# Kernel tuning notes

Hardware: AMD Instinct MI355X
Metric: run time of the kernel (lower is better)

The kernel has to match this reference:

```python
import jax, jax.numpy as jnp
import numpy as np

DIM = 2048   # token width; == heads*head_dim
H, DH = 16, 128
B, S = 1, 2048
E, K = 4, 2          # routed experts, top-k
HID = 5632           # per-expert SwiGLU hidden: round256(int(2*(4*DIM)/3))
HS = 2816            # shared expert hidden: round256(int(2*(2*DIM)/3))


def setup_inputs() -> dict:
    key = jax.random.key(0)
    ks = jax.random.split(key, 24)
    def g(i, shape, s=0.02):
        return jax.random.normal(ks[i], shape, dtype=jnp.float32) * s
    return {
        "image_tokens": jax.random.normal(ks[0], (B, S, DIM), dtype=jnp.float32),
        "adaln_input": jax.random.normal(ks[1], (B, DIM), dtype=jnp.float32),
        "W_ada": g(2, (DIM, 6 * DIM)), "b_ada": g(3, (6 * DIM,)),
        "Wq": g(4, (DIM, DIM)), "bq": g(5, (DIM,)),
        "Wk": g(6, (DIM, DIM)), "bk": g(7, (DIM,)),
        "Wv": g(8, (DIM, DIM)), "bv": g(9, (DIM,)),
        "q_rms_w": jnp.ones((DIM,), jnp.float32) + g(10, (DIM,)),
        "k_rms_w": jnp.ones((DIM,), jnp.float32) + g(11, (DIM,)),
        "Wo": g(12, (DIM, DIM)), "bo": g(13, (DIM,)),
        "gate_w": g(14, (E, DIM)),
        "We1": g(15, (E, DIM, HID)), "We3": g(16, (E, DIM, HID)), "We2": g(17, (E, HID, DIM)),
        "Ws1": g(18, (DIM, HS)), "Ws3": g(19, (DIM, HS)), "Ws2": g(20, (HS, DIM)),
    }


def _ln(x):  # LayerNorm, elementwise_affine=False, eps=1e-6
    m = jnp.mean(x, -1, keepdims=True)
    v = jnp.var(x, -1, keepdims=True)
    return (x - m) * jax.lax.rsqrt(v + 1e-6)


def _rms(x, w):  # RMSNorm with affine weight, eps=1e-5
    return x * jax.lax.rsqrt(jnp.mean(x * x, -1, keepdims=True) + 1e-5) * w


def reference(image_tokens, adaln_input, W_ada, b_ada, Wq, bq, Wk, bk, Wv, bv,
              q_rms_w, k_rms_w, Wo, bo, gate_w, We1, We3, We2, Ws1, Ws3, Ws2):
    # adaLN: SiLU -> Linear -> 6 chunks, each broadcast as [B,1,dim]
    mod = (jax.nn.silu(adaln_input) @ W_ada + b_ada)[:, None, :]
    sh_msa, sc_msa, g_msa, sh_mlp, sc_mlp, g_mlp = jnp.split(mod, 6, axis=-1)

    # attention branch
    x = _ln(image_tokens) * (1.0 + sc_msa) + sh_msa
    q = _rms(x @ Wq + bq, q_rms_w).reshape(B, S, H, DH)
    k = _rms(x @ Wk + bk, k_rms_w).reshape(B, S, H, DH)
    v = (x @ Wv + bv).reshape(B, S, H, DH)
    att = jax.nn.softmax(jnp.einsum('bihd,bjhd->bhij', q, k) / jnp.sqrt(jnp.float32(DH)), axis=-1)
    o = jnp.einsum('bhij,bjhd->bihd', att, v).reshape(B, S, DIM) @ Wo + bo
    img = g_msa * o + image_tokens

    # MoE SwiGLU FFN branch
    y = _ln(img) * (1.0 + sc_mlp) + sh_mlp
    xf = y.reshape(-1, DIM)                                   # [N, dim]
    scores = jax.nn.softmax(xf @ gate_w.T, axis=-1)           # [N, E]
    tw, ti = jax.lax.top_k(scores, K)                         # no top-k renorm (norm_topk_prob=False)
    comb = jnp.zeros((xf.shape[0], E), xf.dtype).at[jnp.arange(xf.shape[0])[:, None], ti].add(tw)
    h = jax.nn.silu(jnp.einsum('nd,edh->neh', xf, We1)) * jnp.einsum('nd,edh->neh', xf, We3)
    routed = jnp.einsum('neh,ehd,ne->nd', h, We2, comb)
    shared = (jax.nn.silu(xf @ Ws1) * (xf @ Ws3)) @ Ws2
    ff = (routed + shared).reshape(B, S, DIM)

    return g_mlp * ff + img
```

## Files before the change

kernel.cpp:

```cpp
#include <hip/hip_runtime.h>
#include <hip/hip_bf16.h>

typedef unsigned short u16;
typedef __bf16 bf16x8 __attribute__((ext_vector_type(8)));
typedef float f32x4 __attribute__((ext_vector_type(4)));
typedef unsigned short u16x8 __attribute__((ext_vector_type(8)));

constexpr int DIMC = 2048;
constexpr int SEQ = 2048;
constexpr int NHEAD = 16;
constexpr int HDIM = 128;
constexpr int NEXP = 4;
constexpr int HIDC = 5632;
constexpr int HSH = 2816;
constexpr int MOD6 = 6 * DIMC;
constexpr int RSTRIDE = 2304;

static __device__ __forceinline__ u16 f2bf(float f) {
  __hip_bfloat16 b = __float2bfloat16(f);
  return __builtin_bit_cast(u16, b);
}
static __device__ __forceinline__ float bf2f(u16 u) {
  unsigned int x = ((unsigned int)u) << 16;
  return __builtin_bit_cast(float, x);
// ... 52 lines not shown
    u16 h, l;
    splitf(v, h, l);
    size_t idx = (size_t)(c0 + ty + i) * R + r0 + tx;
    outh[idx] = h;
    outl[idx] = l;
  }
}

__global__ __launch_bounds__(256) void k_adaln_p(const float* __restrict__ a, const float* __restrict__ W,
                                                 float* __restrict__ partial) {
  __shared__ float sa[128];
  int tid = threadIdx.x, slice = blockIdx.y;
  if (tid < 128) { float v = a[slice * 128 + tid]; sa[tid] = v * sigf(v); }
  __syncthreads();
  int j = blockIdx.x * 256 + tid;
  float acc = 0.f;
#pragma unroll 4
  for (int d = 0; d < 128; ++d) acc += sa[d] * W[(size_t)(slice * 128 + d) * MOD6 + j];
  partial[(size_t)slice * MOD6 + j] = acc;
}
__global__ __launch_bounds__(256) void k_adaln_r(const float* __restrict__ partial, const float* __restrict__ b,
                                                 float* __restrict__ mod) {
  int j = blockIdx.x * 256 + threadIdx.x;
  float acc = b[j];
#pragma unroll
  for (int s = 0; s < 16; ++s) acc += partial[(size_t)s * MOD6 + j];
  mod[j] = acc;
}

__global__ __launch_bounds__(256) void k_ln_mod_split(const float* __restrict__ X, const float* __restrict__ mod,
                                                      int shOff, int scOff, u16* __restrict__ outh,
                                                      u16* __restrict__ outl) {
  int row = blockIdx.x, tid = threadIdx.x;
  const float4* x4 = (const float4*)(X + (size_t)row * DIMC);
  float4 v0 = x4[tid * 2], v1 = x4[tid * 2 + 1];
  float s = v0.x + v0.y + v0.z + v0.w + v1.x + v1.y + v1.z + v1.w;
  float ss = v0.x * v0.x + v0.y * v0.y + v0.z * v0.z + v0.w * v0.w +
             v1.x * v1.x + v1.y * v1.y + v1.z * v1.z + v1.w * v1.w;
  s = blockSum(s);
  ss = blockSum(ss);
  float mean = s * (1.f / DIMC);
  float var = ss * (1.f / DIMC) - mean * mean;
  float rstd = rsqrtf(var + 1e-6f);
  const float* sh = mod + shOff;
  const float* sc = mod + scOff;
  int c = tid * 8;
  float xv[8] = {v0.x, v0.y, v0.z, v0.w, v1.x, v1.y, v1.z, v1.w};
  u16x8 oh, ol;
#pragma unroll
  for (int e = 0; e < 8; ++e) {
    float v = (xv[e] - mean) * rstd * (1.f + sc[c + e]) + sh[c + e];
    u16 h, l;
    splitf(v, h, l);
    oh[e] = h;
    ol[e] = l;
  }
  *(u16x8*)(outh + (size_t)row * DIMC + c) = oh;
  *(u16x8*)(outl + (size_t)row * DIMC + c) = ol;
}

__global__ __launch_bounds__(256) void k_ln_mod(const float* __restrict__ X, const float* __restrict__ mod,
                                                int shOff, int scOff, u16* __restrict__ out) {
  int row = blockIdx.x, tid = threadIdx.x;
  const float4* x4 = (const float4*)(X + (size_t)row * DIMC);
  float4 v0 = x4[tid * 2], v1 = x4[tid * 2 + 1];
  float s = v0.x + v0.y + v0.z + v0.w + v1.x + v1.y + v1.z + v1.w;
  float ss = v0.x * v0.x + v0.y * v0.y + v0.z * v0.z + v0.w * v0.w +
             v1.x * v1.x + v1.y * v1.y + v1.z * v1.z + v1.w * v1.w;
  s = blockSum(s);
  ss = blockSum(ss);
  float mean = s * (1.f / DIMC);
  float var = ss * (1.f / DIMC) - mean * mean;
  float rstd = rsqrtf(var + 1e-6f);
  const float* sh = mod + shOff;
  const float* sc = mod + scOff;
  int c = tid * 8;
  float xv[8] = {v0.x, v0.y, v0.z, v0.w, v1.x, v1.y, v1.z, v1.w};
  u16x8 o;
#pragma unroll
  for (int e = 0; e < 8; ++e) o[e] = f2bf((xv[e] - mean) * rstd * (1.f + sc[c + e]) + sh[c + e]);
  *(u16x8*)(out + (size_t)row * DIMC + c) = o;
}

__global__ __launch_bounds__(256) void k_rms_split(const float* __restrict__ X, const float* __restrict__ w,
                                                   float scale, u16* __restrict__ outh,
                                                   u16* __restrict__ outl) {
  int row = blockIdx.x, tid = threadIdx.x;
  const float4* x4 = (const float4*)(X + (size_t)row * DIMC);
  float4 v0 = x4[tid * 2], v1 = x4[tid * 2 + 1];
  float ss = v0.x * v0.x + v0.y * v0.y + v0.z * v0.z + v0.w * v0.w +
             v1.x * v1.x + v1.y * v1.y + v1.z * v1.z + v1.w * v1.w;
  ss = blockSum(ss);
  float rstd = rsqrtf(ss * (1.f / DIMC) + 1e-5f) * scale;
  int c = tid * 8;
  float xv[8] = {v0.x, v0.y, v0.z, v0.w, v1.x, v1.y, v1.z, v1.w};
  u16x8 oh, ol;
#pragma unroll
  for (int e = 0; e < 8; ++e) {
    float v = xv[e] * rstd * w[c + e];
    u16 h, l;
    splitf(v, h, l);
    oh[e] = h;
    ol[e] = l;
  }
  *(u16x8*)(outh + (size_t)row * DIMC + c) = oh;
  *(u16x8*)(outl + (size_t)row * DIMC + c) = ol;
}

__global__ __launch_bounds__(256) void k_gate(const float* __restrict__ img, const float* __restrict__ mod,
                                              const float* __restrict__ gw, float* __restrict__ comb) {
  int n = blockIdx.x, tid = threadIdx.x;
  const float4* x4 = (const float4*)(img + (size_t)n * DIMC);
  float4 v0 = x4[tid * 2], v1 = x4[tid * 2 + 1];
  float s = v0.x + v0.y + v0.z + v0.w + v1.x + v1.y + v1.z + v1.w;
  float ss = v0.x * v0.x + v0.y * v0.y + v0.z * v0.z + v0.w * v0.w +
             v1.x * v1.x + v1.y * v1.y + v1.z * v1.z + v1.w * v1.w;
  s = blockSum(s);
  ss = blockSum(ss);
  float mean = s * (1.f / DIMC);
  float var = ss * (1.f / DIMC) - mean * mean;
  float rstd = rsqrtf(var + 1e-6f);
  const float* sh = mod + 3 * DIMC;
  const float* sc = mod + 4 * DIMC;
  int c = tid * 8;
  float xv[8] = {v0.x, v0.y, v0.z, v0.w, v1.x, v1.y, v1.z, v1.w};
  float y[8];
#pragma unroll
  for (int e = 0; e < 8; ++e) y[e] = (xv[e] - mean) * rstd * (1.f + sc[c + e]) + sh[c + e];
  float accs[NEXP];
#pragma unroll
  for (int ex = 0; ex < NEXP; ++ex) {
    float a = 0.f;
#pragma unroll
    for (int e = 0; e < 8; ++e) a += y[e] * gw[(size_t)ex * DIMC + c + e];
    accs[ex] = blockSum(a);
  }
  if (tid == 0) {
    float mx = fmaxf(fmaxf(accs[0], accs[1]), fmaxf(accs[2], accs[3]));
    float ex0 = __expf(accs[0] - mx), ex1 = __expf(accs[1] - mx);
    float ex2 = __expf(accs[2] - mx), ex3 = __expf(accs[3] - mx);
    float inv = 1.f / (ex0 + ex1 + ex2 + ex3);
    float v[4] = {ex0 * inv, ex1 * inv, ex2 * inv, ex3 * inv};
    int i1 = 0;
    for (int e = 1; e < 4; ++e)
      if (v[e] > v[i1]) i1 = e;
    int i2 = -1;
    for (int e = 0; e < 4; ++e) {
      if (e == i1) continue;
      if (i2 < 0 || v[e] > v[i2]) i2 = e;
    }
    for (int e = 0; e < 4; ++e) comb[(size_t)n * 4 + e] = (e == i1 || e == i2) ? v[e] : 0.f;
  }
}

__global__ __launch_bounds__(256) void k_route(const float* __restrict__ comb, int* __restrict__ gidx,
                                               float* __restrict__ cw, int* __restrict__ Mpad) {
  int wid = threadIdx.x >> 6, lane = threadIdx.x & 63;
  int base = 0;
  for (int c = 0; c < SEQ; c += 64) {
    int n = c + lane;
    float w = comb[(size_t)n * NEXP + wid];
    bool sel = w > 0.f;
    unsigned long long mask = __ballot(sel);
    int pos = __popcll(mask & ((1ull << lane) - 1ull));
    if (sel) {
      gidx[wid * RSTRIDE + base + pos] = n;
      cw[wid * RSTRIDE + base + pos] = w;
    }
    base += __popcll(mask);
  }
  int padded = (base + 127) & ~127;
  for (int i = base + lane; i < padded; i += 64) {
    gidx[wid * RSTRIDE + i] = -1;
    cw[wid * RSTRIDE + i] = 0.f;
  }
  if (lane == 0) Mpad[wid] = padded;
}

template <int MODE>
__global__ __launch_bounds__(256, 2) void k_gemm(const u16* __restrict__ A, const u16* __restrict__ BT,
                                                 int M, int N, int K, float* __restrict__ Cf,
                                                 u16* __restrict__ Cb, const u16* __restrict__ h1) {
  __shared__ __align__(16) u16 As[2][8192], Bs[2][8192];
  const int tid = threadIdx.x, wid = tid >> 6, lane = tid & 63;
  const int l16 = lane & 15, g = lane >> 4;
  const int wr = wid >> 1, wc = wid & 1;
  const int m0 = blockIdx.y * 128, n0 = blockIdx.x * 128;
  const int srow = lane >> 2, scol = (lane & 3) * 8;
  const u16* aS0 = A + (size_t)(m0 + wid * 32 + srow) * K + scol;
  const u16* aS1 = aS0 + (size_t)16 * K;
  const u16* bS0 = BT + (size_t)(n0 + wid * 32 + srow) * K + scol;
  const u16* bS1 = bS0 + (size_t)16 * K;

  const f32x4 zero4 = {0.f, 0.f, 0.f, 0.f};
  f32x4 acc[4][4];
#pragma unroll
  for (int mi = 0; mi < 4; ++mi)
#pragma unroll
    for (int ni = 0; ni < 4; ++ni) acc[mi][ni] = zero4;

  auto stage = [&](int b, int k0) {
    gload16(aS0 + k0, &As[b][wid * 1024]);
    gload16(aS1 + k0, &As[b][wid * 1024 + 512]);
    gload16(aS0 + k0 + 32, &As[b][4096 + wid * 1024]);
    gload16(aS1 + k0 + 32, &As[b][4096 + wid * 1024 + 512]);
    gload16(bS0 + k0, &Bs[b][wid * 1024]);
    gload16(bS1 + k0, &Bs[b][wid * 1024 + 512]);
    gload16(bS0 + k0 + 32, &Bs[b][4096 + wid * 1024]);
    gload16(bS1 + k0 + 32, &Bs[b][4096 + wid * 1024 + 512]);
  };
  auto compute = [&](int b) {
#pragma unroll
    for (int hh = 0; hh < 2; ++hh) {
      const u16* Asrc = &As[b][hh * 4096];
      const u16* Bsrc = &Bs[b][hh * 4096];
      bf16x8 af[4], bfr[4];
#pragma unroll
      for (int mi = 0; mi < 4; ++mi)
        af[mi] = *(const bf16x8*)(&Asrc[(wr * 64 + mi * 16 + l16) * 32 + g * 8]);
#pragma unroll
      for (int ni = 0; ni < 4; ++ni)
        bfr[ni] = *(const bf16x8*)(&Bsrc[(wc * 64 + ni * 16 + l16) * 32 + g * 8]);
#pragma unroll
      for (int mi = 0; mi < 4; ++mi)
#pragma unroll
        for (int ni = 0; ni < 4; ++ni)
          acc[mi][ni] = __builtin_amdgcn_mfma_f32_16x16x32_bf16(af[mi], bfr[ni], acc[mi][ni], 0, 0, 0);
    }
  };

  stage(0, 0);
  __syncthreads();
  for (int k0 = 0; k0 < K; k0 += 128) {
    if (k0 + 64 < K) stage(1, k0 + 64);
    compute(0);
    __syncthreads();
    if (k0 + 128 < K) stage(0, k0 + 128);
    compute(1);
    __syncthreads();
  }

#pragma unroll
  for (int mi = 0; mi < 4; ++mi) {
#pragma unroll
    for (int ni = 0; ni < 4; ++ni) {
      const int col = n0 + wc * 64 + ni * 16 + l16;
#pragma unroll
      for (int r = 0; r < 4; ++r) {
        const int row = m0 + wr * 64 + mi * 16 + g * 4 + r;
        const size_t idx = (size_t)row * N + col;
        float v = acc[mi][ni][r];
        if constexpr (MODE == 0) {
          Cf[idx] = v;
        } else if constexpr (MODE == 1) {
          Cb[idx] = f2bf(v);
        } else {
          float hv = bf2f(h1[idx]);
          float sw = hv * sigf(hv);
          Cb[idx] = f2bf(sw * v);
        }
      }
    }
  }
}

template <int RM>
__global__ __launch_bounds__(256, 2) void k_gemmR(const u16* __restrict__ A0, size_t az,
                                                  const u16* __restrict__ BT0, size_t bz, int N, int K,
                                                  const int* __restrict__ gidx0,
                                                  const float* __restrict__ cw0,
                                                  const int* __restrict__ Mp0, u16* __restrict__ Cb0,
                                                  size_t cz, const u16* __restrict__ h10,
                                                  float* __restrict__ ff) {
  const int z = blockIdx.z;
  const int* gidxE = gidx0 + (size_t)z * RSTRIDE;
  const int m0 = blockIdx.y * 128;
  if (m0 >= Mp0[z]) return;
  const float* cwE = cw0 + (size_t)z * RSTRIDE;
  const u16* A = A0 + (size_t)z * az;
  const u16* BT = BT0 + (size_t)z * bz;
  u16* Cb = Cb0 + (size_t)z * cz;
  const u16* h1 = h10 + (size_t)z * cz;

  __shared__ __align__(16) u16 As[2][8192], Bs[2][8192];
  const int tid = threadIdx.x, wid = tid >> 6, lane = tid & 63;
  const int l16 = lane & 15, g = lane >> 4;
  const int wr = wid >> 1, wc = wid & 1;
  const int n0 = blockIdx.x * 128;
  const int srow = lane >> 2, scol = (lane & 3) * 8;
  const int slot0 = m0 + wid * 32 + srow;
  int row0, row1;
  if constexpr (RM == 2) {
    row0 = slot0;
    row1 = slot0 + 16;
  } else {
    int t0 = gidxE[slot0], t1 = gidxE[slot0 + 16];
    row0 = t0 < 0 ? 0 : t0;
    row1 = t1 < 0 ? 0 : t1;
  }
  const u16* aS0 = A + (size_t)row0 * K + scol;
  const u16* aS1 = A + (size_t)row1 * K + scol;
  const u16* bS0 = BT + (size_t)(n0 + wid * 32 + srow) * K + scol;
  const u16* bS1 = bS0 + (size_t)16 * K;

  const f32x4 zero4 = {0.f, 0.f, 0.f, 0.f};
  f32x4 acc[4][4];
#pragma unroll
  for (int mi = 0; mi < 4; ++mi)
#pragma unroll
    for (int ni = 0; ni < 4; ++ni) acc[mi][ni] = zero4;

  auto stage = [&](int b, int k0) {
    gload16(aS0 + k0, &As[b][wid * 1024]);
    gload16(aS1 + k0, &As[b][wid * 1024 + 512]);
    gload16(aS0 + k0 + 32, &As[b][4096 + wid * 1024]);
    gload16(aS1 + k0 + 32, &As[b][4096 + wid * 1024 + 512]);
    gload16(bS0 + k0, &Bs[b][wid * 1024]);
    gload16(bS1 + k0, &Bs[b][wid * 1024 + 512]);
    gload16(bS0 + k0 + 32, &Bs[b][4096 + wid * 1024]);
    gload16(bS1 + k0 + 32, &Bs[b][4096 + wid * 1024 + 512]);
  };
  auto compute = [&](int b) {
#pragma unroll
    for (int hh = 0; hh < 2; ++hh) {
      const u16* Asrc = &As[b][hh * 4096];
      const u16* Bsrc = &Bs[b][hh * 4096];
      bf16x8 af[4], bfr[4];
#pragma unroll
      for (int mi = 0; mi < 4; ++mi)
        af[mi] = *(const bf16x8*)(&Asrc[(wr * 64 + mi * 16 + l16) * 32 + g * 8]);
#pragma unroll
      for (int ni = 0; ni < 4; ++ni)
        bfr[ni] = *(const bf16x8*)(&Bsrc[(wc * 64 + ni * 16 + l16) * 32 + g * 8]);
#pragma unroll
      for (int mi = 0; mi < 4; ++mi)
#pragma unroll
        for (int ni = 0; ni < 4; ++ni)
          acc[mi][ni] = __builtin_amdgcn_mfma_f32_16x16x32_bf16(af[mi], bfr[ni], acc[mi][ni], 0, 0, 0);
    }
  };

  stage(0, 0);
  __syncthreads();
  for (int k0 = 0; k0 < K; k0 += 128) {
    if (k0 + 64 < K) stage(1, k0 + 64);
    compute(0);
    __syncthreads();
    if (k0 + 128 < K) stage(0, k0 + 128);
    compute(1);
    __syncthreads();
  }

#pragma unroll
  for (int mi = 0; mi < 4; ++mi) {
#pragma unroll
    for (int ni = 0; ni < 4; ++ni) {
      const int col = n0 + wc * 64 + ni * 16 + l16;
#pragma unroll
      for (int r = 0; r < 4; ++r) {
        const int slot = m0 + wr * 64 + mi * 16 + g * 4 + r;
        const size_t idx = (size_t)slot * N + col;
        float v = acc[mi][ni][r];
        if constexpr (RM == 0) {
          Cb[idx] = f2bf(v);
        } else if constexpr (RM == 1) {
          float hv = bf2f(h1[idx]);
          float sw = hv * sigf(hv);
          Cb[idx] = f2bf(sw * v * cwE[slot]);
        } else {
          int t = gidxE[slot];
          if (t >= 0) ff[(size_t)t * N + col] += v;
        }
      }
    }
  }
}

template <int MODE>
__global__ __launch_bounds__(256, 2) void k_gemm3s(const u16* __restrict__ Ahg, const u16* __restrict__ Alg,
                                                   const u16* __restrict__ Bhg, const u16* __restrict__ Blg,
                                                   int M, int N, int K, float* __restrict__ Cf,
                                                   u16* __restrict__ Ch, u16* __restrict__ Cl,
                                                   const float* __restrict__ bias,
                                                   const float* __restrict__ gvec,
                                                   const float* __restrict__ resid) {
  __shared__ __align__(16) u16 Ahs[2][4096], Als[2][4096], Bhs[2][4096], Bls[2][4096];
  const int tid = threadIdx.x, wid = tid >> 6, lane = tid & 63;
  const int l16 = lane & 15, g = lane >> 4;
  const int wr = wid >> 1, wc = wid & 1;
  const int m0 = blockIdx.y * 128, n0 = blockIdx.x * 128;
  const int srow = lane >> 2, scol = (lane & 3) * 8;
  const size_t aOff0 = (size_t)(m0 + wid * 32 + srow) * K + scol;
  const size_t aOff1 = aOff0 + (size_t)16 * K;
  const size_t bOff0 = (size_t)(n0 + wid * 32 + srow) * K + scol;
  const size_t bOff1 = bOff0 + (size_t)16 * K;

  const f32x4 zero4 = {0.f, 0.f, 0.f, 0.f};
  f32x4 acc[4][4];
#pragma unroll
  for (int mi = 0; mi < 4; ++mi)
#pragma unroll
    for (int ni = 0; ni < 4; ++ni) acc[mi][ni] = zero4;

  auto stage = [&](int b, int k0) {
    gload16(Ahg + aOff0 + k0, &Ahs[b][wid * 1024]);
    gload16(Ahg + aOff1 + k0, &Ahs[b][wid * 1024 + 512]);
    gload16(Alg + aOff0 + k0, &Als[b][wid * 1024]);
    gload16(Alg + aOff1 + k0, &Als[b][wid * 1024 + 512]);
    gload16(Bhg + bOff0 + k0, &Bhs[b][wid * 1024]);
    gload16(Bhg + bOff1 + k0, &Bhs[b][wid * 1024 + 512]);
    gload16(Blg + bOff0 + k0, &Bls[b][wid * 1024]);
    gload16(Blg + bOff1 + k0, &Bls[b][wid * 1024 + 512]);
  };
  auto compute = [&](int b) {
    bf16x8 bhf[4], blf[4];
#pragma unroll
    for (int ni = 0; ni < 4; ++ni) {
      bhf[ni] = *(const bf16x8*)(&Bhs[b][(wc * 64 + ni * 16 + l16) * 32 + g * 8]);
      blf[ni] = *(const bf16x8*)(&Bls[b][(wc * 64 + ni * 16 + l16) * 32 + g * 8]);
    }
#pragma unroll
    for (int mi = 0; mi < 4; ++mi) {
      bf16x8 ahf = *(const bf16x8*)(&Ahs[b][(wr * 64 + mi * 16 + l16) * 32 + g * 8]);
      bf16x8 alf = *(const bf16x8*)(&Als[b][(wr * 64 + mi * 16 + l16) * 32 + g * 8]);
#pragma unroll
      for (int ni = 0; ni < 4; ++ni) {
        acc[mi][ni] = __builtin_amdgcn_mfma_f32_16x16x32_bf16(alf, bhf[ni], acc[mi][ni], 0, 0, 0);
        acc[mi][ni] = __builtin_amdgcn_mfma_f32_16x16x32_bf16(ahf, blf[ni], acc[mi][ni], 0, 0, 0);
        acc[mi][ni] = __builtin_amdgcn_mfma_f32_16x16x32_bf16(ahf, bhf[ni], acc[mi][ni], 0, 0, 0);
      }
    }
  };

  stage(0, 0);
  __syncthreads();
  for (int k0 = 0; k0 < K; k0 += 64) {
    if (k0 + 32 < K) stage(1, k0 + 32);
    compute(0);
    __syncthreads();
    if (k0 + 64 < K) stage(0, k0 + 64);
    compute(1);
    __syncthreads();
  }

#pragma unroll
  for (int mi = 0; mi < 4; ++mi) {
#pragma unroll
    for (int ni = 0; ni < 4; ++ni) {
      const int col = n0 + wc * 64 + ni * 16 + l16;
      float bv = bias ? bias[col] : 0.f;
#pragma unroll
      for (int r = 0; r < 4; ++r) {
        const int row = m0 + wr * 64 + mi * 16 + g * 4 + r;
        float v = acc[mi][ni][r] + bv;
        if constexpr (MODE == 0) {
          Cf[(size_t)row * N + col] = v;
        } else if constexpr (MODE == 2) {
          Cf[(size_t)row * N + col] = v * gvec[col] + resid[(size_t)row * N + col];
        } else {
          u16 h, l;
          splitf(v, h, l);
          Ch[(size_t)col * M + row] = h;
          Cl[(size_t)col * M + row] = l;
        }
      }
    }
  }
}

__global__ __launch_bounds__(256, 3) void k_flash3(const u16* __restrict__ qh_g, const u16* __restrict__ ql_g,
                                                   const u16* __restrict__ kh_g, const u16* __restrict__ kl_g,
                                                   const u16* __restrict__ vth_g, const u16* __restrict__ vtl_g,
                                                   u16* __restrict__ oh_g, u16* __restrict__ ol_g) {
  __shared__ __align__(16) u16 Kh[4096], Kl[4096], Vh[128 * 40], Vl[128 * 40];
  __shared__ __align__(16) u16 Pah[4][16 * 40], Pal[4][16 * 40];
  const int tid = threadIdx.x, wid = tid >> 6, lane = tid & 63;
  const int l16 = lane & 15, g = lane >> 4;
  const int h = blockIdx.y;
  const int r0 = blockIdx.x * 64 + wid * 16;
  const size_t hOff = (size_t)h * HDIM;

  bf16x8 qfh[4], qfl[4];
#pragma unroll
  for (int kc = 0; kc < 4; ++kc) {
    const size_t qo = (size_t)(r0 + l16) * DIMC + hOff + kc * 32 + g * 8;
    qfh[kc] = *(const bf16x8*)(qh_g + qo);
    qfl[kc] = *(const bf16x8*)(ql_g + qo);
  }

  const int kr = tid >> 3, ke0 = (tid & 7) * 16;
  const int kswz = (kr & 7) << 4;
  const int kc0 = (ke0 * 2) ^ kswz, kc1 = (ke0 * 2 + 16) ^ kswz;
  char* khp = (char*)Kh + kr * 256;
  char* klp = (char*)Kl + kr * 256;
  const size_t kOff = (size_t)kr * DIMC + hOff + ke0;
  const int vr = tid >> 1, ve0 = (tid & 1) * 16;
  char* vhp = (char*)Vh + vr * 80 + ve0 * 2;
  char* vlp = (char*)Vl + vr * 80 + ve0 * 2;
  const size_t vOff = (size_t)(hOff + vr) * SEQ + ve0;

  u16x8 kH0, kH1, kL0, kL1, vH0, vH1, vL0, vL1;
  kH0 = *(const u16x8*)(kh_g + kOff);
  kH1 = *(const u16x8*)(kh_g + kOff + 8);
  kL0 = *(const u16x8*)(kl_g + kOff);
  kL1 = *(const u16x8*)(kl_g + kOff + 8);
  vH0 = *(const u16x8*)(vth_g + vOff);
  vH1 = *(const u16x8*)(vth_g + vOff + 8);
  vL0 = *(const u16x8*)(vtl_g + vOff);
  vL1 = *(const u16x8*)(vtl_g + vOff + 8);

  const f32x4 zero4 = {0.f, 0.f, 0.f, 0.f};
  f32x4 oacc[8];
#pragma unroll
  for (int db = 0; db < 8; ++db) oacc[db] = zero4;
  float mr[4], lr[4];
#pragma unroll
  for (int r = 0; r < 4; ++r) {
    mr[r] = -3.0e38f;
    lr[r] = 0.f;
  }

  for (int j0 = 0; j0 < SEQ; j0 += 32) {
    __syncthreads();
    *(u16x8*)(khp + kc0) = kH0;
    *(u16x8*)(khp + kc1) = kH1;
    *(u16x8*)(klp + kc0) = kL0;
    *(u16x8*)(klp + kc1) = kL1;
    *(u16x8*)(vhp) = vH0;
    *(u16x8*)(vhp + 16) = vH1;
    *(u16x8*)(vlp) = vL0;
    *(u16x8*)(vlp + 16) = vL1;
    __syncthreads();
    if (j0 + 32 < SEQ) {
      const size_t ko = kOff + (size_t)(j0 + 32) * DIMC;
      const size_t vo = vOff + j0 + 32;
      kH0 = *(const u16x8*)(kh_g + ko);
      kH1 = *(const u16x8*)(kh_g + ko + 8);
      kL0 = *(const u16x8*)(kl_g + ko);
      kL1 = *(const u16x8*)(kl_g + ko + 8);
      vH0 = *(const u16x8*)(vth_g + vo);
      vH1 = *(const u16x8*)(vth_g + vo + 8);
      vL0 = *(const u16x8*)(vtl_g + vo);
      vL1 = *(const u16x8*)(vtl_g + vo + 8);
    }
    f32x4 s0 = zero4, s1 = zero4;
    __builtin_amdgcn_s_setprio(1);
#pragma unroll
    for (int kc = 0; kc < 4; ++kc) {
      const int cb = (kc * 64 + g * 16) ^ ((l16 & 7) << 4);
      bf16x8 kh0 = *(const bf16x8*)((char*)Kh + l16 * 256 + cb);
// ... 41 lines not shown
      oacc[db] = __builtin_amdgcn_mfma_f32_16x16x32_bf16(pfl, vh, oacc[db], 0, 0, 0);
      oacc[db] = __builtin_amdgcn_mfma_f32_16x16x32_bf16(pfh, vl, oacc[db], 0, 0, 0);
      oacc[db] = __builtin_amdgcn_mfma_f32_16x16x32_bf16(pfh, vh, oacc[db], 0, 0, 0);
    }
    __builtin_amdgcn_s_setprio(0);
  }
#pragma unroll
  for (int r = 0; r < 4; ++r) {
#pragma unroll
    for (int m = 1; m < 16; m <<= 1) lr[r] += __shfl_xor(lr[r], m);
    lr[r] = 1.f / lr[r];
  }
#pragma unroll
  for (int db = 0; db < 8; ++db)
#pragma unroll
    for (int r = 0; r < 4; ++r) {
      float v = oacc[db][r] * lr[r];
      u16 hh, ll;
      splitf(v, hh, ll);
      const size_t idx = (size_t)(r0 + g * 4 + r) * DIMC + hOff + db * 16 + l16;
      oh_g[idx] = hh;
      ol_g[idx] = ll;
    }
}

__global__ __launch_bounds__(256) void k_final(const float* __restrict__ ff, const float* img,
                                               const float* __restrict__ mod, float* out) {
  const float4* gm = (const float4*)(mod + 5 * DIMC);
  const int total = SEQ * DIMC / 4;
  const int stride = gridDim.x * blockDim.x;
  for (int i = blockIdx.x * blockDim.x + threadIdx.x; i < total; i += stride) {
    int col4 = i & (DIMC / 4 - 1);
    float4 gv = gm[col4];
    float4 fv = ((const float4*)ff)[i];
    float4 iv = ((const float4*)img)[i];
    float4 ov;
    ov.x = gv.x * fv.x + iv.x;
    ov.y = gv.y * fv.y + iv.y;
    ov.z = gv.z * fv.z + iv.z;
    ov.w = gv.w * fv.w + iv.w;
    ((float4*)out)[i] = ov;
  }
}

extern "C" void kernel_launch(void* const* d_in, const int* in_sizes, int n_in, void* d_out, int out_size,
                              void* d_ws, size_t ws_size, hipStream_t stream) {
  (void)in_sizes; (void)n_in; (void)out_size; (void)ws_size;
  const float* image_tokens = (const float*)d_in[0];
  const float* adaln_input = (const float*)d_in[1];
  const float* W_ada = (const float*)d_in[2];
  const float* b_ada = (const float*)d_in[3];
  const float* Wq = (const float*)d_in[4];
  const float* bq = (const float*)d_in[5];
  const float* Wk = (const float*)d_in[6];
  const float* bk = (const float*)d_in[7];
  const float* Wv = (const float*)d_in[8];
  const float* bv = (const float*)d_in[9];
  const float* q_rms_w = (const float*)d_in[10];
  const float* k_rms_w = (const float*)d_in[11];
  const float* Wo = (const float*)d_in[12];
  const float* bo = (const float*)d_in[13];
  const float* gate_w = (const float*)d_in[14];
  const float* We1 = (const float*)d_in[15];
  const float* We3 = (const float*)d_in[16];
  const float* We2 = (const float*)d_in[17];
  const float* Ws1 = (const float*)d_in[18];
  const float* Ws3 = (const float*)d_in[19];
  const float* Ws2 = (const float*)d_in[20];

  char* cur = (char*)d_ws;
  auto alloc = [&](size_t n) {
    char* p = cur;
    cur += (n + 255) & ~(size_t)255;
    return p;
  };
  float* modv = (float*)alloc((size_t)MOD6 * 4);
  float* adap = (float*)alloc((size_t)16 * MOD6 * 4);
  float* comb = (float*)alloc((size_t)SEQ * NEXP * 4);
  int* gidx = (int*)alloc((size_t)NEXP * RSTRIDE * 4);
  float* cw = (float*)alloc((size_t)NEXP * RSTRIDE * 4);
  int* Mpad = (int*)alloc((size_t)NEXP * 4);
  u16* xh = (u16*)alloc((size_t)SEQ * DIMC * 2);
  u16* xl = (u16*)alloc((size_t)SEQ * DIMC * 2);
  u16* wTh = (u16*)alloc((size_t)DIMC * DIMC * 2);
  u16* wTl = (u16*)alloc((size_t)DIMC * DIMC * 2);
  float* tf = (float*)alloc((size_t)SEQ * DIMC * 4);
  u16* qhb = (u16*)alloc((size_t)SEQ * DIMC * 2);
  u16* qlb = (u16*)alloc((size_t)SEQ * DIMC * 2);
  u16* khb = (u16*)alloc((size_t)SEQ * DIMC * 2);
  u16* klb = (u16*)alloc((size_t)SEQ * DIMC * 2);
  u16* vth = (u16*)alloc((size_t)SEQ * DIMC * 2);
  u16* vtl = (u16*)alloc((size_t)SEQ * DIMC * 2);
  u16* aoh = (u16*)alloc((size_t)SEQ * DIMC * 2);
  u16* aol = (u16*)alloc((size_t)SEQ * DIMC * 2);
  u16* x_act = (u16*)alloc((size_t)SEQ * DIMC * 2);
  float* ff = (float*)alloc((size_t)SEQ * DIMC * 4);
  float* img = (float*)d_out;
  u16* wbufE = xh;
  u16* H1G2 = (u16*)((char*)xh + (size_t)2 * HIDC * DIMC * 2);
  const size_t BZ = (size_t)HIDC * DIMC;
  const size_t CZ = (size_t)RSTRIDE * HIDC;
  u16* wbufS = wbufE;
  u16* H1Gs = H1G2;

  dim3 blk(256);
  auto gemm3s = [&](int mode, const u16* Ah, const u16* Al, int M, int N, int K, float* Cf, u16* Ch,
                    u16* Cl, const float* bias, const float* gv, const float* resid) {
    dim3 grid(N / 128, M / 128);
    switch (mode) {
      case 0:
        k_gemm3s<0><<<grid, blk, 0, stream>>>(Ah, Al, wTh, wTl, M, N, K, Cf, Ch, Cl, bias, gv, resid);
        break;
      case 2:
        k_gemm3s<2><<<grid, blk, 0, stream>>>(Ah, Al, wTh, wTl, M, N, K, Cf, Ch, Cl, bias, gv, resid);
        break;
      default:
        k_gemm3s<6><<<grid, blk, 0, stream>>>(Ah, Al, wTh, wTl, M, N, K, Cf, Ch, Cl, bias, gv, resid);
        break;
    }
  };

  k_adaln_p<<<dim3(MOD6 / 256, 16), blk, 0, stream>>>(adaln_input, W_ada, adap);
  k_adaln_r<<<dim3(MOD6 / 256), blk, 0, stream>>>(adap, b_ada, modv);

  k_ln_mod_split<<<dim3(SEQ), blk, 0, stream>>>(image_tokens, modv, 0, DIMC, xh, xl);
  k_transpose_s<<<dim3(DIMC / 32, DIMC / 32), blk, 0, stream>>>(Wq, wTh, wTl, DIMC, DIMC, DIMC);
  gemm3s(0, xh, xl, SEQ, DIMC, DIMC, tf, nullptr, nullptr, bq, nullptr, nullptr);
  k_rms_split<<<dim3(SEQ), blk, 0, stream>>>(tf, q_rms_w, 0.08838834764831845f, qhb, qlb);
  k_transpose_s<<<dim3(DIMC / 32, DIMC / 32), blk, 0, stream>>>(Wk, wTh, wTl, DIMC, DIMC, DIMC);
  gemm3s(0, xh, xl, SEQ, DIMC, DIMC, tf, nullptr, nullptr, bk, nullptr, nullptr);
  k_rms_split<<<dim3(SEQ), blk, 0, stream>>>(tf, k_rms_w, 1.f, khb, klb);
  k_transpose_s<<<dim3(DIMC / 32, DIMC / 32), blk, 0, stream>>>(Wv, wTh, wTl, DIMC, DIMC, DIMC);
  gemm3s(6, xh, xl, SEQ, DIMC, DIMC, nullptr, vth, vtl, bv, nullptr, nullptr);
  k_flash3<<<dim3(SEQ / 64, NHEAD), blk, 0, stream>>>(qhb, qlb, khb, klb, vth, vtl, aoh, aol);
  k_transpose_s<<<dim3(DIMC / 32, DIMC / 32), blk, 0, stream>>>(Wo, wTh, wTl, DIMC, DIMC, DIMC);
  gemm3s(2, aoh, aol, SEQ, DIMC, DIMC, img, nullptr, nullptr, bo, modv + 2 * DIMC, image_tokens);

  k_ln_mod<<<dim3(SEQ), blk, 0, stream>>>(img, modv, 3 * DIMC, 4 * DIMC, x_act);
  k_gate<<<dim3(SEQ), blk, 0, stream>>>(img, modv, gate_w, comb);
  k_route<<<dim3(1), blk, 0, stream>>>(comb, gidx, cw, Mpad);

  k_transpose<<<dim3(HSH / 32, DIMC / 32), blk, 0, stream>>>(Ws1, wbufS, DIMC, HSH, HSH, 0, 0);
  k_gemm<1><<<dim3(HSH / 128, SEQ / 128), blk, 0, stream>>>(x_act, wbufS, SEQ, HSH, DIMC, nullptr,
                                                            H1Gs, nullptr);
  k_transpose<<<dim3(HSH / 32, DIMC / 32), blk, 0, stream>>>(Ws3, wbufS, DIMC, HSH, HSH, 0, 0);
  k_gemm<3><<<dim3(HSH / 128, SEQ / 128), blk, 0, stream>>>(x_act, wbufS, SEQ, HSH, DIMC, nullptr,
                                                            H1Gs, H1Gs);
  k_transpose<<<dim3(DIMC / 32, HSH / 32), blk, 0, stream>>>(Ws2, wbufS, HSH, DIMC, DIMC, 0, 0);
  k_gemm<0><<<dim3(DIMC / 128, SEQ / 128), blk, 0, stream>>>(H1Gs, wbufS, SEQ, DIMC, HSH, ff,
                                                             nullptr, nullptr);

  const size_t WE = (size_t)DIMC * HIDC;
  for (int p = 0; p < 2; ++p) {
    const int e0 = p * 2;
    const int* ge = gidx + e0 * RSTRIDE;
    const float* ce = cw + e0 * RSTRIDE;
    const int* me = Mpad + e0;
    k_transpose<<<dim3(HIDC / 32, DIMC / 32, 2), blk, 0, stream>>>(We1 + (size_t)e0 * WE, wbufE,
                                                                   DIMC, HIDC, HIDC, WE, BZ);
    k_gemmR<0><<<dim3(HIDC / 128, SEQ / 128, 2), blk, 0, stream>>>(x_act, 0, wbufE, BZ, HIDC, DIMC,
                                                                   ge, ce, me, H1G2, CZ, H1G2, nullptr);
    k_transpose<<<dim3(HIDC / 32, DIMC / 32, 2), blk, 0, stream>>>(We3 + (size_t)e0 * WE, wbufE,
                                                                   DIMC, HIDC, HIDC, WE, BZ);
    k_gemmR<1><<<dim3(HIDC / 128, SEQ / 128, 2), blk, 0, stream>>>(x_act, 0, wbufE, BZ, HIDC, DIMC,
                                                                   ge, ce, me, H1G2, CZ, H1G2, nullptr);
    k_transpose<<<dim3(DIMC / 32, HIDC / 32, 2), blk, 0, stream>>>(We2 + (size_t)e0 * WE, wbufE,
                                                                   HIDC, DIMC, DIMC, WE, BZ);
    for (int z = 0; z < 2; ++z) {
      k_gemmR<2><<<dim3(DIMC / 128, SEQ / 128, 1), blk, 0, stream>>>(
          H1G2 + (size_t)z * CZ, 0, wbufE + (size_t)z * BZ, 0, DIMC, HIDC, gidx + (e0 + z) * RSTRIDE,
          cw + (e0 + z) * RSTRIDE, Mpad + e0 + z, H1G2, 0, H1G2, ff);
    }
  }

  k_final<<<dim3(1024), blk, 0, stream>>>(ff, img, modv, (float*)d_out);
}
```

Measured before the change: 1.715 ms.

## Fuse QKV projection into one GEMM and fuse SwiGLU up-projections into dual-B GEMM

Transposes Wq/Wk/Wv into one concatenated buffer and runs a single 3-split GEMM over N=3*DIM with a per-column-block bias select. RMS norms then read strided rows from the fused output, and V is transposed by a separate kernel. The gate/up GEMMs for both the shared and routed experts become one kernel that loads A once and accumulates against W1 and W3 together, applying SiLU-multiply and the routing weight in the epilogue. This saves A reloads, kernel launches and the bf16 H1 round trip through memory. In exchange the fused kernel keeps twice the accumulators and drops double-buffered staging, which may cut occupancy and latency hiding, and the QKV output buffer triples in size.

```diff
diff --git a/kernel.cpp b/kernel.cpp
--- a/kernel.cpp
+++ b/kernel.cpp
@@ -158,11 +158,11 @@
   *(u16x8*)(out + (size_t)row * DIMC + c) = o;
 }
 
-__global__ __launch_bounds__(256) void k_rms_split(const float* __restrict__ X, const float* __restrict__ w,
-                                                   float scale, u16* __restrict__ outh,
-                                                   u16* __restrict__ outl) {
+__global__ __launch_bounds__(256) void k_rms_split(const float* __restrict__ X, int ldin,
+                                                   const float* __restrict__ w, float scale,
+                                                   u16* __restrict__ outh, u16* __restrict__ outl) {
   int row = blockIdx.x, tid = threadIdx.x;
-  const float4* x4 = (const float4*)(X + (size_t)row * DIMC);
+  const float4* x4 = (const float4*)(X + (size_t)row * ldin);
   float4 v0 = x4[tid * 2], v1 = x4[tid * 2 + 1];
   float ss = v0.x * v0.x + v0.y * v0.y + v0.z * v0.z + v0.w * v0.w +
              v1.x * v1.x + v1.y * v1.y + v1.z * v1.z + v1.w * v1.w;
@@ -253,10 +253,8 @@
   if (lane == 0) Mpad[wid] = padded;
 }
 
-template <int MODE>
-__global__ __launch_bounds__(256, 2) void k_gemm(const u16* __restrict__ A, const u16* __restrict__ BT,
-                                                 int M, int N, int K, float* __restrict__ Cf,
-                                                 u16* __restrict__ Cb, const u16* __restrict__ h1) {
+__global__ __launch_bounds__(256, 2) void k_gemmD(const u16* __restrict__ A, const u16* __restrict__ BT,
+                                                  int M, int N, int K, float* __restrict__ Cf) {
   __shared__ __align__(16) u16 As[2][8192], Bs[2][8192];
   const int tid = threadIdx.x, wid = tid >> 6, lane = tid & 63;
   const int l16 = lane & 15, g = lane >> 4;
@@ -317,47 +315,132 @@
   }
 
 #pragma unroll
-  for (int mi = 0; mi < 4; ++mi) {
+  for (int mi = 0; mi < 4; ++mi)
 #pragma unroll
     for (int ni = 0; ni < 4; ++ni) {
       const int col = n0 + wc * 64 + ni * 16 + l16;
 #pragma unroll
       for (int r = 0; r < 4; ++r) {
         const int row = m0 + wr * 64 + mi * 16 + g * 4 + r;
-        const size_t idx = (size_t)row * N + col;
-        float v = acc[mi][ni][r];
-        if constexpr (MODE == 0) {
-          Cf[idx] = v;
-        } else if constexpr (MODE == 1) {
-          Cb[idx] = f2bf(v);
-        } else {
-          float hv = bf2f(h1[idx]);
-          float sw = hv * sigf(hv);
-          Cb[idx] = f2bf(sw * v);
+        Cf[(size_t)row * N + col] = acc[mi][ni][r];
+      }
+    }
+}
+
+template <int GATH>
+__global__ __launch_bounds__(256, 2) void k_gemmUP(const u16* __restrict__ A, const u16* __restrict__ B1T0,
+                                                   const u16* __restrict__ B3T0, size_t bz, int N, int K,
+                                                   const int* __restrict__ gidx0,
+                                                   const float* __restrict__ cw0,
+                                                   const int* __restrict__ Mp0, u16* __restrict__ G0,
+                                                   size_t cz) {
+  const int z = blockIdx.z;
+  const int m0 = blockIdx.y * 128;
+  const int* gidxE = nullptr;
+  const float* cwE = nullptr;
+  if constexpr (GATH) {
+    if (m0 >= Mp0[z]) return;
+    gidxE = gidx0 + (size_t)z * RSTRIDE;
+    cwE = cw0 + (size_t)z * RSTRIDE;
+  }
+  const u16* B1T = B1T0 + (size_t)z * bz;
+  const u16* B3T = B3T0 + (size_t)z * bz;
+  u16* G = G0 + (size_t)z * cz;
+
+  __shared__ __align__(16) u16 As[8192], B1s[8192], B3s[8192];
+  const int tid = threadIdx.x, wid = tid >> 6, lane = tid & 63;
+  const int l16 = lane & 15, g = lane >> 4;
+  const int wr = wid >> 1, wc = wid & 1;
+  const int n0 = blockIdx.x * 128;
+  const int srow = lane >> 2, scol = (lane & 3) * 8;
+  const int slot0 = m0 + wid * 32 + srow;
+  int row0, row1;
+  if constexpr (GATH) {
+    int t0 = gidxE[slot0], t1 = gidxE[slot0 + 16];
+    row0 = t0 < 0 ? 0 : t0;
+    row1 = t1 < 0 ? 0 : t1;
+  } else {
+    row0 = slot0;
+    row1 = slot0 + 16;
+  }
+  const u16* aS0 = A + (size_t)row0 * K + scol;
+  const u16* aS1 = A + (size_t)row1 * K + scol;
+  const u16* b1S0 = B1T + (size_t)(n0 + wid * 32 + srow) * K + scol;
+  const u16* b1S1 = b1S0 + (size_t)16 * K;
+  const u16* b3S0 = B3T + (size_t)(n0 + wid * 32 + srow) * K + scol;
+  const u16* b3S1 = b3S0 + (size_t)16 * K;
+
+  const f32x4 zero4 = {0.f, 0.f, 0.f, 0.f};
+  f32x4 acc1[4][4], acc3[4][4];
+#pragma unroll
+  for (int mi = 0; mi < 4; ++mi)
+#pragma unroll
+    for (int ni = 0; ni < 4; ++ni) {
+      acc1[mi][ni] = zero4;
+      acc3[mi][ni] = zero4;
+    }
+
+  for (int k0 = 0; k0 < K; k0 += 64) {
+    __syncthreads();
+    gload16(aS0 + k0, &As[wid * 1024]);
+    gload16(aS1 + k0, &As[wid * 1024 + 512]);
+    gload16(aS0 + k0 + 32, &As[4096 + wid * 1024]);
+    gload16(aS1 + k0 + 32, &As[4096 + wid * 1024 + 512]);
+    gload16(b1S0 + k0, &B1s[wid * 1024]);
+    gload16(b1S1 + k0, &B1s[wid * 1024 + 512]);
+    gload16(b1S0 + k0 + 32, &B1s[4096 + wid * 1024]);
+    gload16(b1S1 + k0 + 32, &B1s[4096 + wid * 1024 + 512]);
+    gload16(b3S0 + k0, &B3s[wid * 1024]);
+    gload16(b3S1 + k0, &B3s[wid * 1024 + 512]);
+    gload16(b3S0 + k0 + 32, &B3s[4096 + wid * 1024]);
+    gload16(b3S1 + k0 + 32, &B3s[4096 + wid * 1024 + 512]);
+    __syncthreads();
+#pragma unroll
+    for (int hh = 0; hh < 2; ++hh) {
+      const u16* Asrc = &As[hh * 4096];
+      const u16* B1src = &B1s[hh * 4096];
+      const u16* B3src = &B3s[hh * 4096];
+      bf16x8 af[4], b1f[4], b3f[4];
+#pragma unroll
+      for (int mi = 0; mi < 4; ++mi)
+        af[mi] = *(const bf16x8*)(&Asrc[(wr * 64 + mi * 16 + l16) * 32 + g * 8]);
+#pragma unroll
+      for (int ni = 0; ni < 4; ++ni) {
+        b1f[ni] = *(const bf16x8*)(&B1src[(wc * 64 + ni * 16 + l16) * 32 + g * 8]);
+        b3f[ni] = *(const bf16x8*)(&B3src[(wc * 64 + ni * 16 + l16) * 32 + g * 8]);
+      }
+#pragma unroll
+      for (int mi = 0; mi < 4; ++mi)
+#pragma unroll
+        for (int ni = 0; ni < 4; ++ni) {
+          acc1[mi][ni] = __builtin_amdgcn_mfma_f32_16x16x32_bf16(af[mi], b1f[ni], acc1[mi][ni], 0, 0, 0);
+          acc3[mi][ni] = __builtin_amdgcn_mfma_f32_16x16x32_bf16(af[mi], b3f[ni], acc3[mi][ni], 0, 0, 0);
         }
+    }
+  }
+
+#pragma unroll
+  for (int mi = 0; mi < 4; ++mi)
+#pragma unroll
+    for (int ni = 0; ni < 4; ++ni) {
+      const int col = n0 + wc * 64 + ni * 16 + l16;
+#pragma unroll
+      for (int r = 0; r < 4; ++r) {
+        const int slot = m0 + wr * 64 + mi * 16 + g * 4 + r;
+        float hv = bf2f(f2bf(acc1[mi][ni][r]));
+        float sw = hv * sigf(hv);
+        float val = sw * acc3[mi][ni][r];
+        if constexpr (GATH) val = val * cwE[slot];
+        G[(size_t)slot * N + col] = f2bf(val);
       }
     }
-  }
-}
-
-template <int RM>
-__global__ __launch_bounds__(256, 2) void k_gemmR(const u16* __restrict__ A0, size_t az,
-                                                  const u16* __restrict__ BT0, size_t bz, int N, int K,
-                                                  const int* __restrict__ gidx0,
-                                                  const float* __restrict__ cw0,
-                                                  const int* __restrict__ Mp0, u16* __restrict__ Cb0,
-                                                  size_t cz, const u16* __restrict__ h10,
-                                                  float* __restrict__ ff) {
-  const int z = blockIdx.z;
-  const int* gidxE = gidx0 + (size_t)z * RSTRIDE;
+}
+
+__global__ __launch_bounds__(256, 2) void k_gemmR2(const u16* __restrict__ A, const u16* __restrict__ BT,
+                                                   int N, int K, const int* __restrict__ gidxE,
+                                                   const int* __restrict__ MpE, float* __restrict__ ff) {
   const int m0 = blockIdx.y * 128;
-  if (m0 >= Mp0[z]) return;
-  const float* cwE = cw0 + (size_t)z * RSTRIDE;
-  const u16* A = A0 + (size_t)z * az;
-  const u16* BT = BT0 + (size_t)z * bz;
-  u16* Cb = Cb0 + (size_t)z * cz;
-  const u16* h1 = h10 + (size_t)z * cz;
-
+  if (m0 >= *MpE) return;
   __shared__ __align__(16) u16 As[2][8192], Bs[2][8192];
   const int tid = threadIdx.x, wid = tid >> 6, lane = tid & 63;
   const int l16 = lane & 15, g = lane >> 4;
@@ -365,17 +448,8 @@
   const int n0 = blockIdx.x * 128;
   const int srow = lane >> 2, scol = (lane & 3) * 8;
   const int slot0 = m0 + wid * 32 + srow;
-  int row0, row1;
-  if constexpr (RM == 2) {
-    row0 = slot0;
-    row1 = slot0 + 16;
-  } else {
-    int t0 = gidxE[slot0], t1 = gidxE[slot0 + 16];
-    row0 = t0 < 0 ? 0 : t0;
-    row1 = t1 < 0 ? 0 : t1;
-  }
-  const u16* aS0 = A + (size_t)row0 * K + scol;
-  const u16* aS1 = A + (size_t)row1 * K + scol;
+  const u16* aS0 = A + (size_t)slot0 * K + scol;
+  const u16* aS1 = A + (size_t)(slot0 + 16) * K + scol;
   const u16* bS0 = BT + (size_t)(n0 + wid * 32 + srow) * K + scol;
   const u16* bS1 = bS0 + (size_t)16 * K;
 
@@ -428,36 +502,26 @@
   }
 
 #pragma unroll
-  for (int mi = 0; mi < 4; ++mi) {
+  for (int mi = 0; mi < 4; ++mi)
 #pragma unroll
     for (int ni = 0; ni < 4; ++ni) {
       const int col = n0 + wc * 64 + ni * 16 + l16;
 #pragma unroll
       for (int r = 0; r < 4; ++r) {
         const int slot = m0 + wr * 64 + mi * 16 + g * 4 + r;
-        const size_t idx = (size_t)slot * N + col;
-        float v = acc[mi][ni][r];
-        if constexpr (RM == 0) {
-          Cb[idx] = f2bf(v);
-        } else if constexpr (RM == 1) {
-          float hv = bf2f(h1[idx]);
-          float sw = hv * sigf(hv);
-          Cb[idx] = f2bf(sw * v * cwE[slot]);
-        } else {
-          int t = gidxE[slot];
-          if (t >= 0) ff[(size_t)t * N + col] += v;
-        }
+        int t = gidxE[slot];
+        if (t >= 0) ff[(size_t)t * N + col] += acc[mi][ni][r];
       }
     }
-  }
 }
 
 template <int MODE>
 __global__ __launch_bounds__(256, 2) void k_gemm3s(const u16* __restrict__ Ahg, const u16* __restrict__ Alg,
                                                    const u16* __restrict__ Bhg, const u16* __restrict__ Blg,
                                                    int M, int N, int K, float* __restrict__ Cf,
-                                                   u16* __restrict__ Ch, u16* __restrict__ Cl,
-                                                   const float* __restrict__ bias,
+                                                   const float* __restrict__ bias0,
+                                                   const float* __restrict__ bias1,
+                                                   const float* __restrict__ bias2,
                                                    const float* __restrict__ gvec,
                                                    const float* __restrict__ resid) {
   __shared__ __align__(16) u16 Ahs[2][4096], Als[2][4096], Bhs[2][4096], Bls[2][4096];
@@ -519,29 +583,25 @@
     __syncthreads();
   }
 
-#pragma unroll
-  for (int mi = 0; mi < 4; ++mi) {
+  const float* bp = bias0;
+  if constexpr (MODE == 7) bp = (n0 < DIMC) ? bias0 : (n0 < 2 * DIMC ? bias1 : bias2);
+#pragma unroll
+  for (int mi = 0; mi < 4; ++mi)
 #pragma unroll
     for (int ni = 0; ni < 4; ++ni) {
       const int col = n0 + wc * 64 + ni * 16 + l16;
-      float bv = bias ? bias[col] : 0.f;
+      float bv = bp ? bp[col & (DIMC - 1)] : 0.f;
 #pragma unroll
       for (int r = 0; r < 4; ++r) {
         const int row = m0 + wr * 64 + mi * 16 + g * 4 + r;
         float v = acc[mi][ni][r] + bv;
-        if constexpr (MODE == 0) {
+        if constexpr (MODE == 7) {
           Cf[(size_t)row * N + col] = v;
-        } else if constexpr (MODE == 2) {
+        } else {
           Cf[(size_t)row * N + col] = v * gvec[col] + resid[(size_t)row * N + col];
-        } else {
-          u16 h, l;
-          splitf(v, h, l);
-          Ch[(size_t)col * M + row] = h;
-          Cl[(size_t)col * M + row] = l;
         }
       }
     }
-  }
 }
 
 __global__ __launch_bounds__(256, 3) void k_flash3(const u16* __restrict__ qh_g, const u16* __restrict__ ql_g,
@@ -749,9 +809,9 @@
   int* Mpad = (int*)alloc((size_t)NEXP * 4);
   u16* xh = (u16*)alloc((size_t)SEQ * DIMC * 2);
   u16* xl = (u16*)alloc((size_t)SEQ * DIMC * 2);
-  u16* wTh = (u16*)alloc((size_t)DIMC * DIMC * 2);
-  u16* wTl = (u16*)alloc((size_t)DIMC * DIMC * 2);
-  float* tf = (float*)alloc((size_t)SEQ * DIMC * 4);
+  u16* wTh3 = (u16*)alloc((size_t)3 * DIMC * DIMC * 2);
+  u16* wTl3 = (u16*)alloc((size_t)3 * DIMC * DIMC * 2);
+  float* tf3 = (float*)alloc((size_t)SEQ * 3 * DIMC * 4);
   u16* qhb = (u16*)alloc((size_t)SEQ * DIMC * 2);
   u16* qlb = (u16*)alloc((size_t)SEQ * DIMC * 2);
   u16* khb = (u16*)alloc((size_t)SEQ * DIMC * 2);
@@ -763,80 +823,66 @@
   u16* x_act = (u16*)alloc((size_t)SEQ * DIMC * 2);
   float* ff = (float*)alloc((size_t)SEQ * DIMC * 4);
   float* img = (float*)d_out;
-  u16* wbufE = xh;
-  u16* H1G2 = (u16*)((char*)xh + (size_t)2 * HIDC * DIMC * 2);
   const size_t BZ = (size_t)HIDC * DIMC;
   const size_t CZ = (size_t)RSTRIDE * HIDC;
-  u16* wbufS = wbufE;
-  u16* H1Gs = H1G2;
+  u16* moe0 = xh;
+  u16* wbufE1 = moe0;
+  u16* wbufE3 = moe0 + 2 * BZ;
+  u16* G2 = moe0 + 4 * BZ;
+  u16* wbufS1 = moe0;
+  u16* wbufS3 = moe0 + (size_t)HSH * DIMC;
+  u16* wbufS2 = moe0 + (size_t)2 * HSH * DIMC;
+  u16* Gs = moe0 + (size_t)3 * HSH * DIMC;
 
   dim3 blk(256);
-  auto gemm3s = [&](int mode, const u16* Ah, const u16* Al, int M, int N, int K, float* Cf, u16* Ch,
-                    u16* Cl, const float* bias, const float* gv, const float* resid) {
-    dim3 grid(N / 128, M / 128);
-    switch (mode) {
-      case 0:
-        k_gemm3s<0><<<grid, blk, 0, stream>>>(Ah, Al, wTh, wTl, M, N, K, Cf, Ch, Cl, bias, gv, resid);
-        break;
-      case 2:
-        k_gemm3s<2><<<grid, blk, 0, stream>>>(Ah, Al, wTh, wTl, M, N, K, Cf, Ch, Cl, bias, gv, resid);
-        break;
-      default:
-        k_gemm3s<6><<<grid, blk, 0, stream>>>(Ah, Al, wTh, wTl, M, N, K, Cf, Ch, Cl, bias, gv, resid);
-        break;
-    }
-  };
 
   k_adaln_p<<<dim3(MOD6 / 256, 16), blk, 0, stream>>>(adaln_input, W_ada, adap);
   k_adaln_r<<<dim3(MOD6 / 256), blk, 0, stream>>>(adap, b_ada, modv);
 
   k_ln_mod_split<<<dim3(SEQ), blk, 0, stream>>>(image_tokens, modv, 0, DIMC, xh, xl);
-  k_transpose_s<<<dim3(DIMC / 32, DIMC / 32), blk, 0, stream>>>(Wq, wTh, wTl, DIMC, DIMC, DIMC);
-  gemm3s(0, xh, xl, SEQ, DIMC, DIMC, tf, nullptr, nullptr, bq, nullptr, nullptr);
-  k_rms_split<<<dim3(SEQ), blk, 0, stream>>>(tf, q_rms_w, 0.08838834764831845f, qhb, qlb);
-  k_transpose_s<<<dim3(DIMC / 32, DIMC / 32), blk, 0, stream>>>(Wk, wTh, wTl, DIMC, DIMC, DIMC);
-  gemm3s(0, xh, xl, SEQ, DIMC, DIMC, tf, nullptr, nullptr, bk, nullptr, nullptr);
-  k_rms_split<<<dim3(SEQ), blk, 0, stream>>>(tf, k_rms_w, 1.f, khb, klb);
-  k_transpose_s<<<dim3(DIMC / 32, DIMC / 32), blk, 0, stream>>>(Wv, wTh, wTl, DIMC, DIMC, DIMC);
-  gemm3s(6, xh, xl, SEQ, DIMC, DIMC, nullptr, vth, vtl, bv, nullptr, nullptr);
+  k_transpose_s<<<dim3(DIMC / 32, DIMC / 32), blk, 0, stream>>>(Wq, wTh3, wTl3, DIMC, DIMC, DIMC);
+  k_transpose_s<<<dim3(DIMC / 32, DIMC / 32), blk, 0, stream>>>(
+      Wk, wTh3 + (size_t)DIMC * DIMC, wTl3 + (size_t)DIMC * DIMC, DIMC, DIMC, DIMC);
+  k_transpose_s<<<dim3(DIMC / 32, DIMC / 32), blk, 0, stream>>>(
+      Wv, wTh3 + (size_t)2 * DIMC * DIMC, wTl3 + (size_t)2 * DIMC * DIMC, DIMC, DIMC, DIMC);
+  k_gemm3s<7><<<dim3(3 * DIMC / 128, SEQ / 128), blk, 0, stream>>>(
+      xh, xl, wTh3, wTl3, SEQ, 3 * DIMC, DIMC, tf3, bq, bk, bv, nullptr, nullptr);
+  k_rms_split<<<dim3(SEQ), blk, 0, stream>>>(tf3, 3 * DIMC, q_rms_w, 0.08838834764831845f, qhb, qlb);
+  k_rms_split<<<dim3(SEQ), blk, 0, stream>>>(tf3 + DIMC, 3 * DIMC, k_rms_w, 1.f, khb, klb);
+  k_transpose_s<<<dim3(DIMC / 32, SEQ / 32), blk, 0, stream>>>(tf3 + 2 * DIMC, vth, vtl, SEQ, DIMC,
+                                                               3 * DIMC);
   k_flash3<<<dim3(SEQ / 64, NHEAD), blk, 0, stream>>>(qhb, qlb, khb, klb, vth, vtl, aoh, aol);
-  k_transpose_s<<<dim3(DIMC / 32, DIMC / 32), blk, 0, stream>>>(Wo, wTh, wTl, DIMC, DIMC, DIMC);
-  gemm3s(2, aoh, aol, SEQ, DIMC, DIMC, img, nullptr, nullptr, bo, modv + 2 * DIMC, image_tokens);
+  k_transpose_s<<<dim3(DIMC / 32, DIMC / 32), blk, 0, stream>>>(Wo, wTh3, wTl3, DIMC, DIMC, DIMC);
+  k_gemm3s<2><<<dim3(DIMC / 128, SEQ / 128), blk, 0, stream>>>(
+      aoh, aol, wTh3, wTl3, SEQ, DIMC, DIMC, img, bo, nullptr, nullptr, modv + 2 * DIMC, image_tokens);
 
   k_ln_mod<<<dim3(SEQ), blk, 0, stream>>>(img, modv, 3 * DIMC, 4 * DIMC, x_act);
   k_gate<<<dim3(SEQ), blk, 0, stream>>>(img, modv, gate_w, comb);
   k_route<<<dim3(1), blk, 0, stream>>>(comb, gidx, cw, Mpad);
 
-  k_transpose<<<dim3(HSH / 32, DIMC / 32), blk, 0, stream>>>(Ws1, wbufS, DIMC, HSH, HSH, 0, 0);
-  k_gemm<1><<<dim3(HSH / 128, SEQ / 128), blk, 0, stream>>>(x_act, wbufS, SEQ, HSH, DIMC, nullptr,
-                                                            H1Gs, nullptr);
-  k_transpose<<<dim3(HSH / 32, DIMC / 32), blk, 0, stream>>>(Ws3, wbufS, DIMC, HSH, HSH, 0, 0);
-  k_gemm<3><<<dim3(HSH / 128, SEQ / 128), blk, 0, stream>>>(x_act, wbufS, SEQ, HSH, DIMC, nullptr,
-                                                            H1Gs, H1Gs);
-  k_transpose<<<dim3(DIMC / 32, HSH / 32), blk, 0, stream>>>(Ws2, wbufS, HSH, DIMC, DIMC, 0, 0);
-  k_gemm<0><<<dim3(DIMC / 128, SEQ / 128), blk, 0, stream>>>(H1Gs, wbufS, SEQ, DIMC, HSH, ff,
-                                                             nullptr, nullptr);
+  k_transpose<<<dim3(HSH / 32, DIMC / 32), blk, 0, stream>>>(Ws1, wbufS1, DIMC, HSH, HSH, 0, 0);
+  k_transpose<<<dim3(HSH / 32, DIMC / 32), blk, 0, stream>>>(Ws3, wbufS3, DIMC, HSH, HSH, 0, 0);
+  k_gemmUP<0><<<dim3(HSH / 128, SEQ / 128, 1), blk, 0, stream>>>(
+      x_act, wbufS1, wbufS3, 0, HSH, DIMC, nullptr, nullptr, nullptr, Gs, 0);
+  k_transpose<<<dim3(DIMC / 32, HSH / 32), blk, 0, stream>>>(Ws2, wbufS2, HSH, DIMC, DIMC, 0, 0);
+  k_gemmD<<<dim3(DIMC / 128, SEQ / 128), blk, 0, stream>>>(Gs, wbufS2, SEQ, DIMC, HSH, ff);
 
   const size_t WE = (size_t)DIMC * HIDC;
   for (int p = 0; p < 2; ++p) {
     const int e0 = p * 2;
-    const int* ge = gidx + e0 * RSTRIDE;
-    const float* ce = cw + e0 * RSTRIDE;
-    const int* me = Mpad + e0;
-    k_transpose<<<dim3(HIDC / 32, DIMC / 32, 2), blk, 0, stream>>>(We1 + (size_t)e0 * WE, wbufE,
+    k_transpose<<<dim3(HIDC / 32, DIMC / 32, 2), blk, 0, stream>>>(We1 + (size_t)e0 * WE, wbufE1,
                                                                    DIMC, HIDC, HIDC, WE, BZ);
-    k_gemmR<0><<<dim3(HIDC / 128, SEQ / 128, 2), blk, 0, stream>>>(x_act, 0, wbufE, BZ, HIDC, DIMC,
-                                                                   ge, ce, me, H1G2, CZ, H1G2, nullptr);
-    k_transpose<<<dim3(HIDC / 32, DIMC / 32, 2), blk, 0, stream>>>(We3 + (size_t)e0 * WE, wbufE,
+    k_transpose<<<dim3(HIDC / 32, DIMC / 32, 2), blk, 0, stream>>>(We3 + (size_t)e0 * WE, wbufE3,
                                                                    DIMC, HIDC, HIDC, WE, BZ);
-    k_gemmR<1><<<dim3(HIDC / 128, SEQ / 128, 2), blk, 0, stream>>>(x_act, 0, wbufE, BZ, HIDC, DIMC,
-                                                                   ge, ce, me, H1G2, CZ, H1G2, nullptr);
-    k_transpose<<<dim3(DIMC / 32, HIDC / 32, 2), blk, 0, stream>>>(We2 + (size_t)e0 * WE, wbufE,
+    k_gemmUP<1><<<dim3(HIDC / 128, SEQ / 128, 2), blk, 0, stream>>>(
+        x_act, wbufE1, wbufE3, BZ, HIDC, DIMC, gidx + e0 * RSTRIDE, cw + e0 * RSTRIDE, Mpad + e0, G2,
+        CZ);
+    k_transpose<<<dim3(DIMC / 32, HIDC / 32, 2), blk, 0, stream>>>(We2 + (size_t)e0 * WE, wbufE1,
                                                                    HIDC, DIMC, DIMC, WE, BZ);
     for (int z = 0; z < 2; ++z) {
-      k_gemmR<2><<<dim3(DIMC / 128, SEQ / 128, 1), blk, 0, stream>>>(
-          H1G2 + (size_t)z * CZ, 0, wbufE + (size_t)z * BZ, 0, DIMC, HIDC, gidx + (e0 + z) * RSTRIDE,
-          cw + (e0 + z) * RSTRIDE, Mpad + e0 + z, H1G2, 0, H1G2, ff);
+      k_gemmR2<<<dim3(DIMC / 128, SEQ / 128), blk, 0, stream>>>(
+          G2 + (size_t)z * CZ, wbufE1 + (size_t)z * BZ, DIMC, HIDC, gidx + (e0 + z) * RSTRIDE,
+          Mpad + e0 + z, ff);
     }
   }
 
```

After: 1.541 ms. 1.11x faster.
